# Kernel optimization log

Hardware: AMD Instinct MI355X
Metric: run time of the kernel (lower is better)

Reference implementation:

```python
import jax, jax.numpy as jnp
import numpy as np

PI = 3.141592653589793
TAU = 0.5          # gumbel-softmax temperature
EPS = 1e-6
B, N, D = 128, 32, 256

def _linear(x, w, b=None):
    y = x @ w.T
    return y if b is None else y + b

def _wrap(a):
    return (a + PI) % (2 * PI) - PI

def setup_inputs() -> dict:
    key = jax.random.key(0)
    ks = jax.random.split(key, 16)
    s = 0.05
    return {
        "embedding": jax.random.normal(ks[0], (B, N, 11), jnp.float32),
        "gumbel_u": jax.random.uniform(ks[1], (B * N, N - 1, 2), jnp.float32),
        "emb1_w": jax.random.normal(ks[2], (128, 5), jnp.float32) * s,
        "emb1_b": jnp.zeros((128,), jnp.float32),
        "emb2_w": jax.random.normal(ks[3], (D, 128), jnp.float32) * s,
        "emb2_b": jnp.zeros((D,), jnp.float32),
        "hm1_w": jax.random.normal(ks[4], (D, D + 7), jnp.float32) * s,
        "hm1_b": jnp.zeros((D,), jnp.float32),
        "hm2_w": jax.random.normal(ks[5], (D, D), jnp.float32) * s,
        "hm2_b": jnp.zeros((D,), jnp.float32),
        "he_w": jax.random.normal(ks[6], (2, D), jnp.float32) * s,
        "he_b": jnp.zeros((2,), jnp.float32),
        "q_w": jax.random.normal(ks[7], (D, D), jnp.float32) * s,
        "k_w": jax.random.normal(ks[8], (D, 10), jnp.float32) * s,
        "v_w": jax.random.normal(ks[9], (D, 10), jnp.float32) * s,
        "v_b": jnp.zeros((D,), jnp.float32),
        "dec_w": jax.random.normal(ks[10], (2 * D, 2 * D), jnp.float32) * s,
        "dec_b": jnp.zeros((2 * D,), jnp.float32),
    }

def reference(embedding, gumbel_u, emb1_w, emb1_b, emb2_w, emb2_b,
              hm1_w, hm1_b, hm2_w, hm2_b, he_w, he_b,
              q_w, k_w, v_w, v_b, dec_w, dec_b):
    b, n, _ = embedding.shape
    d = q_w.shape[0]
    # static off-diagonal index lists (i,j), j != i, row-major like mask indexing
    rows, cols = np.nonzero(~np.eye(n, dtype=bool))

    embed = embedding[:, :, 4:9].reshape(b * n, 5)
    position = embedding[:, :, :2]
    heading = embedding[:, :, 2:4]
    action = embedding[:, :, 7:9]
    goal = embedding[:, :, -2:]

    # agent embedding MLP (leaky_relu slope 0.01, torch default)
    h = jax.nn.leaky_relu(_linear(embed, emb1_w, emb1_b))
    agent_embed = jax.nn.leaky_relu(_linear(h, emb2_w, emb2_b)).reshape(b, n, d)

    # pairwise geometry  [b,i,j,...]
    rel_vec = position[:, None, :, :] - position[:, :, None, :]   # pos_j - pos_i
    dx, dy = rel_vec[..., 0], rel_vec[..., 1]
    rel_dist = jnp.linalg.norm(rel_vec, axis=-1, keepdims=True) / 12.0
    heading_angle_i = jnp.arctan2(heading[..., 1], heading[..., 0])[:, :, None]  # [b,n,1]
    angle = _wrap(jnp.arctan2(dy, dx) - heading_angle_i)
    hj_cos = jnp.broadcast_to(heading[:, None, :, 0], (b, n, n))
    hj_sin = jnp.broadcast_to(heading[:, None, :, 1], (b, n, n))
    action_j = jnp.broadcast_to(action[:, None, :, :], (b, n, n, 2))
    edge_features = jnp.concatenate([
        rel_dist, jnp.cos(angle)[..., None], jnp.sin(angle)[..., None],
        hj_cos[..., None], hj_sin[..., None], action_j], axis=-1)  # [b,n,n,7]

    # hard attention branch (off-diagonal pairs only)
    h_i_flat = jnp.broadcast_to(agent_embed[:, :, None, :], (b, n, n - 1, d)).reshape(b * n, n - 1, d)
    edge_flat = edge_features[:, rows, cols].reshape(b * n, n - 1, 7)
    hard_input = jnp.concatenate([h_i_flat, edge_flat], axis=-1)
    h_hard = _linear(jax.nn.relu(_linear(hard_input, hm1_w, hm1_b)), hm2_w, hm2_b)
    hard_logits = _linear(h_hard, he_w, he_b)                      # [b*n, n-1, 2]
    g = -jnp.log(-jnp.log(gumbel_u + 1e-10) + 1e-10)
    hard_soft = jax.nn.softmax((hard_logits + g) / TAU, axis=-1)
    hard_weights = hard_soft[..., 1].reshape(b, n, n - 1)

    unnorm = jnp.linalg.norm(rel_vec, axis=-1, keepdims=True)      # [b,n,n,1]
    unnorm_rel_dist = unnorm[:, rows, cols].reshape(b * n, n - 1, 1)

    # goal polar features
    goal_rel_vec = goal[:, None, :, :] - position[:, :, None, :]   # [b,n,n,2]
    goal_rel_dist = jnp.linalg.norm(goal_rel_vec, axis=-1, keepdims=True)
    goal_rel_angle = _wrap(jnp.arctan2(goal_rel_vec[..., 1], goal_rel_vec[..., 0]) - heading_angle_i)
    goal_polar = jnp.concatenate([goal_rel_dist, jnp.cos(goal_rel_angle)[..., None],
                                  jnp.sin(goal_rel_angle)[..., None]], axis=-1)
    soft_edge = jnp.concatenate([edge_features, goal_polar], axis=-1)  # [b,n,n,10]

    # soft attention (vectorized over agents; off-diagonal gather)
    q = agent_embed @ q_w.T                                         # [b,n,d]
    k = soft_edge @ k_w.T                                           # [b,n,n,d]
    v = jax.nn.relu(_linear(soft_edge, v_w, v_b))                   # [b,n,n,d]
    k_off = k[:, rows, cols].reshape(b, n, n - 1, d)
    v_off = v[:, rows, cols].reshape(b, n, n - 1, d)
    score = jnp.einsum('bnd,bnjd->bnj', q, k_off) / jnp.sqrt(jnp.float32(d))
    soft_w = jax.nn.softmax(score, axis=-1)
    combined = soft_w * hard_weights                                # [b,n,n-1]
    x = jnp.einsum('bnjd,bnj->bnd', v_off, combined).reshape(b * n, d)

    final_input = jnp.concatenate([agent_embed.reshape(b * n, d), x], axis=-1)
    output = _linear(final_input, dec_w, dec_b)                     # [b*n, 2d]

    cwn = combined / (combined.sum(axis=-1, keepdims=True) + EPS)
    mean_entropy = (-(cwn * jnp.log(cwn + EPS)).sum(axis=-1)).mean()
    comb_w = combined.reshape(n, -1)  # matches torch.stack(dim=1).reshape(n, -1)

    return (output, hard_logits[..., 1], unnorm_rel_dist, mean_entropy, hard_weights, comb_w)
```

## Files before the change

### kernel.cpp

```cpp
#include <hip/hip_runtime.h>
#include <hip/hip_bf16.h>
#include <math.h>

typedef __hip_bfloat16 bf16;
typedef short bf16x8 __attribute__((ext_vector_type(8)));
typedef float f32x4 __attribute__((ext_vector_type(4)));
typedef unsigned short u16;

#define R_TOT 4096
#define NJ 31

#define OFF_AE   0
#define OFF_QK   1048576
#define OFF_S1   2097152
#define OFF_ENT  4542464
#define OFF_X    4546560
#define OFF_W    5595136
#define W_E1W   0
#define W_E1B   640
#define W_E2P   768
#define W_E2B   33536
#define W_H1W   33792
#define W_H1B   101120
#define W_H2B   166912
#define W_HEW   167168
#define W_HEB   167680
#define W_W1EP  167684
#define W_HE2P  171780
#define W_CB    173828
#define W_S1P   200452
#define W_KW    233220
#define W_VW    235780
#define W_VB    238340
#define W_DECWT 238596
#define W_DECB  500740
#define W_QKM   501252

#define OUT0 0
#define OUT1 2097152
#define OUT2 2224128
#define OUT3 2351104
#define OUT4 2351105
#define OUT5 2478081

__device__ __forceinline__ float b2f(bf16 x) { return __bfloat162float(x); }
__device__ __forceinline__ float ldin(const void* p, int i, int flag) {
    return flag ? b2f(((const bf16*)p)[i]) : ((const float*)p)[i];
}
__device__ __forceinline__ void stout(void* p, int i, float v, int flag) {
    if (flag) ((bf16*)p)[i] = __float2bfloat16(v);
    else      ((float*)p)[i] = v;
}
__device__ __forceinline__ u16 f2bbits(float v) {
    bf16 h = __float2bfloat16(v);
    return *(u16*)&h;
}
__device__ __forceinline__ int detect_flag(const void* emb) {
    float x = ((const float*)emb)[threadIdx.x & 63];
    int sane = (x == x) && (fabsf(x) < 1e20f);
    unsigned long long m = __ballot(sane);
    return (__popcll(m) == 64) ? 0 : 1;
}

__global__ __launch_bounds__(256) void k_prep(
        const void* emb,
        const void* e1w, const void* e1b, const void* e2w, const void* e2b,
        const void* h1w, const void* h1b, const void* h2w, const void* h2b,
        const void* hew, const void* heb, const void* qw,  const void* kw,
        const void* vw,  const void* vb,  const void* decw,const void* decb,
        float* W) {
    int flag = detect_flag(emb);
    int blk = blockIdx.x;
    if (blk < 2048) {
        int idx = blk * 256 + threadIdx.x;
        if (idx < 262144) {
            int jj   = idx & 7;
            int lane = (idx >> 3) & 63;
            int tile = idx >> 9;
            int nt = tile & 31, kt = tile >> 5;
            int n = nt * 16 + (lane & 15);
            int k = kt * 32 + ((lane >> 4) << 3) + jj;
            ((u16*)(W + W_DECWT))[idx] = f2bbits(ldin(decw, n * 512 + k, flag));
        }
        int j = idx - 262144;
        if (j >= 0 && j < 98304) {
            int p;
            const void* src; int ldm, Wdst;
            if (j < 32768)      { p = j;          src = e2w; ldm = 128; Wdst = W_E2P; }
            else                { p = j - 32768;  src = h1w; ldm = 263; Wdst = W_S1P; }
            int jj   = p & 7;
            int lane = (p >> 3) & 63;
            int tile = p >> 9;
            int nt = tile & 15, kt = tile >> 4;
            int n = nt * 16 + (lane & 15);
            int k = kt * 32 + ((lane >> 4) << 3) + jj;
            ((u16*)(W + Wdst))[p] = f2bbits(ldin(src, n * ldm + k, flag));
        } else if (j >= 98304 && j < 174082) {
            int q2 = j - 98304;
            if      (q2 < 640)   W[W_E1W  + q2]           = ldin(e1w,  q2,          flag);
            else if (q2 < 768)   W[W_E1B  + (q2 - 640)]   = ldin(e1b,  q2 - 640,    flag);
            else if (q2 < 1024)  W[W_E2B  + (q2 - 768)]   = ldin(e2b,  q2 - 768,    flag);
            else if (q2 < 68352) W[W_H1W  + (q2 - 1024)]  = ldin(h1w,  q2 - 1024,   flag);
            else if (q2 < 68608) W[W_H1B  + (q2 - 68352)] = ldin(h1b,  q2 - 68352,  flag);
            else if (q2 < 68864) W[W_H2B  + (q2 - 68608)] = ldin(h2b,  q2 - 68608,  flag);
            else if (q2 < 69376) W[W_HEW  + (q2 - 68864)] = ldin(hew,  q2 - 68864,  flag);
            else if (q2 < 69378) W[W_HEB  + (q2 - 69376)] = ldin(heb,  q2 - 69376,  flag);
            else if (q2 < 71938) W[W_KW   + (q2 - 69378)] = ldin(kw,   q2 - 69378,  flag);
            else if (q2 < 74498) W[W_VW   + (q2 - 71938)] = ldin(vw,   q2 - 71938,  flag);
            else if (q2 < 74754) W[W_VB   + (q2 - 74498)] = ldin(vb,   q2 - 74498,  flag);
            else                 W[W_DECB + (q2 - 74754)] = ldin(decb, q2 - 74754,  flag);
        }
    } else if (blk < 2064) {
        int p = (blk - 2048) * 256 + threadIdx.x;
        int jj = p & 7, lane = (p >> 3) & 63, kt = p >> 9;
        int k = kt * 32 + ((lane >> 4) << 3) + jj;
        int n = lane & 15;
        float v = 0.f;
        if (n < 10) {
            for (int d = 0; d < 256; d++)
                v += ldin(qw, d * 256 + k, flag) * ldin(kw, d * 10 + n, flag);
        }
        ((u16*)(W + W_QKM))[p] = f2bbits(v);
    } else {
        int p = (blk - 2064) * 256 + threadIdx.x;
        if (p < 8192) {
            int jj = p & 7, lane = (p >> 3) & 63, nt = p >> 9;
            int n = nt * 16 + (lane & 15);
            int k = ((lane >> 4) << 3) + jj;
            float v = (k < 7) ? ldin(h1w, n * 263 + 256 + k, flag) : 0.f;
            ((u16*)(W + W_W1EP))[p] = f2bbits(v);
        } else if (p < 12288) {
            int q = p - 8192;
            int jj = q & 7, lane = (q >> 3) & 63, kt = q >> 9;
            int n = lane & 15;
            int c = kt * 32 + ((lane >> 4) << 3) + jj;
            float v = 0.f;
            if (n < 2) {
                for (int d = 0; d < 256; d++)
                    v += ldin(hew, n * 256 + d, flag) * ldin(h2w, d * 256 + c, flag);
            }
            ((u16*)(W + W_HE2P))[q] = f2bbits(v);
        } else if (p < 12290) {
            int i = p - 12288;
            float v = ldin(heb, i, flag);
            for (int d = 0; d < 256; d++)
                v += ldin(hew, i * 256 + d, flag) * ldin(h2b, d, flag);
            W[W_CB + i] = v;
        }
    }
}

__global__ __launch_bounds__(256) void k_embed(const void* emb, const float* W,
                                               u16* aeb, float* qkws, float* s1ws) {
    int flag = detect_flag(emb);
    int r0 = blockIdx.x * 16;
    __shared__ float embL[16][12];
    __shared__ u16 hB[16][136];
    __shared__ u16 aeB[16][264];
    int tid = threadIdx.x;
    for (int idx = tid; idx < 16 * 11; idx += 256) {
        int s = idx / 11, t = idx % 11;
        embL[s][t] = ldin(emb, (r0 + s) * 11 + t, flag);
    }
    __syncthreads();
    for (int idx = tid; idx < 16 * 128; idx += 256) {
        int s = idx >> 7, jo = idx & 127;
        float v = W[W_E1B + jo];
#pragma unroll
        for (int t = 0; t < 5; t++) v += W[W_E1W + jo * 5 + t] * embL[s][4 + t];
        hB[s][jo] = f2bbits(v > 0.f ? v : 0.01f * v);
    }
    __syncthreads();
    int wv = tid >> 6, ln = tid & 63;
    int lr = ln & 15, quad = ln >> 4;
    {
        const bf16x8* Bp = (const bf16x8*)(W + W_E2P);
        f32x4 acc[4];
#pragma unroll
        for (int nt = 0; nt < 4; nt++) acc[nt] = (f32x4){0.f, 0.f, 0.f, 0.f};
#pragma unroll
        for (int kt = 0; kt < 4; kt++) {
            bf16x8 af = *(const bf16x8*)&hB[lr][kt * 32 + (quad << 3)];
#pragma unroll
            for (int nt = 0; nt < 4; nt++) {
                bf16x8 bfr = Bp[(kt * 16 + (wv * 4 + nt)) * 64 + ln];
                acc[nt] = __builtin_amdgcn_mfma_f32_16x16x32_bf16(af, bfr, acc[nt], 0, 0, 0);
            }
        }
#pragma unroll
        for (int nt = 0; nt < 4; nt++) {
            int d = wv * 64 + nt * 16 + lr;
            float bias = W[W_E2B + d];
#pragma unroll
            for (int reg = 0; reg < 4; reg++) {
                int m = quad * 4 + reg;
                float v = acc[nt][reg] + bias;
                v = v > 0.f ? v : 0.01f * v;
                u16 bits = f2bbits(v);
                aeB[m][d] = bits;
                aeb[(r0 + m) * 256 + d] = bits;
            }
        }
    }
    __syncthreads();
    {
        const bf16x8* Bs = (const bf16x8*)(W + W_S1P);
        f32x4 sac[4];
#pragma unroll
        for (int nt = 0; nt < 4; nt++) sac[nt] = (f32x4){0.f, 0.f, 0.f, 0.f};
#pragma unroll
        for (int kt = 0; kt < 8; kt++) {
            bf16x8 af = *(const bf16x8*)&aeB[lr][kt * 32 + (quad << 3)];
#pragma unroll
            for (int nt = 0; nt < 4; nt++) {
                bf16x8 bs = Bs[(kt * 16 + (wv * 4 + nt)) * 64 + ln];
                sac[nt] = __builtin_amdgcn_mfma_f32_16x16x32_bf16(af, bs, sac[nt], 0, 0, 0);
            }
        }
#pragma unroll
        for (int nt = 0; nt < 4; nt++) {
            int d = wv * 64 + nt * 16 + lr;
            float bias = W[W_H1B + d];
#pragma unroll
            for (int reg = 0; reg < 4; reg++) {
                int m = quad * 4 + reg;
                s1ws[(r0 + m) * 256 + d] = sac[nt][reg] + bias;
            }
        }
        if (wv == 0) {
            const bf16x8* Bm = (const bf16x8*)(W + W_QKM);
            f32x4 qk = (f32x4){0.f, 0.f, 0.f, 0.f};
#pragma unroll
            for (int kt = 0; kt < 8; kt++) {
                bf16x8 af = *(const bf16x8*)&aeB[lr][kt * 32 + (quad << 3)];
                qk = __builtin_amdgcn_mfma_f32_16x16x32_bf16(af, Bm[kt * 64 + ln], qk, 0, 0, 0);
            }
            if (lr < 10) {
#pragma unroll
                for (int reg = 0; reg < 4; reg++) {
                    int m = quad * 4 + reg;
                    qkws[(r0 + m) * 10 + lr] = qk[reg];
                }
            }
        }
    }
}

__global__ __launch_bounds__(256) void k_fused(const void* emb, const void* gum,
                                               const float* s1ws, const float* qkws, const float* W,
                                               u16* xb, float* entws, void* out) {
    int flag = detect_flag(emb);
    int r = blockIdx.x;
    int b = r >> 5, i = r & 31;
    __shared__ float embB[32][12];
    __shared__ float seL[32][10];
    __shared__ u16 eA[32][32];
    __shared__ u16 a1[32][264];
    __shared__ float pj[4][32][2];
    __shared__ float cL[32];
    __shared__ float qkL[10];
    int tid = threadIdx.x;
    for (int idx = tid; idx < 32 * 11; idx += 256) {
        int s = idx / 11, t = idx % 11;
        embB[s][t] = ldin(emb, (b * 32 + s) * 11 + t, flag);
    }
    for (int idx = tid; idx < 32 * 32; idx += 256) ((u16*)eA)[idx] = 0;
    if (tid >= 64 && tid < 74) qkL[tid - 64] = qkws[r * 10 + (tid - 64)];
    __syncthreads();
    if (tid < NJ) {
        int jp = tid;
        int j = jp + (jp >= i ? 1 : 0);
        float pix = embB[i][0], piy = embB[i][1], hix = embB[i][2], hiy = embB[i][3];
        float pjx = embB[j][0], pjy = embB[j][1], hjx = embB[j][2], hjy = embB[j][3];
        float ajx = embB[j][7], ajy = embB[j][8];
        float gjx = embB[j][9], gjy = embB[j][10];
        float dx = pjx - pix, dy = pjy - piy;
        float dist = sqrtf(dx * dx + dy * dy);
        float hai = atan2f(hiy, hix);
        float ang = atan2f(dy, dx) - hai;
        float gx = gjx - pix, gy = gjy - piy;
        float gdist = sqrtf(gx * gx + gy * gy);
        float gang = atan2f(gy, gx) - hai;
        float f[10];
        f[0] = dist * (1.f / 12.f);
        f[1] = cosf(ang); f[2] = sinf(ang);
        f[3] = hjx; f[4] = hjy; f[5] = ajx; f[6] = ajy;
        f[7] = gdist; f[8] = cosf(gang); f[9] = sinf(gang);
#pragma unroll
        for (int t = 0; t < 10; t++) seL[jp][t] = f[t];
#pragma unroll
        for (int t = 0; t < 7; t++) eA[jp][t] = f2bbits(f[t]);
        stout(out, OUT2 + r * NJ + jp, dist, flag);
    }
    __syncthreads();
    int wv = tid >> 6, ln = tid & 63;
    int lr = ln & 15, quad = ln >> 4;
    {
        const bf16x8* Bp = (const bf16x8*)(W + W_W1EP);
        bf16x8 af0 = *(const bf16x8*)&eA[lr][quad << 3];
        bf16x8 af1 = *(const bf16x8*)&eA[16 + lr][quad << 3];
#pragma unroll
        for (int nt = 0; nt < 4; nt++) {
            int gnt = wv * 4 + nt;
            int d = gnt * 16 + lr;
            float s1v = s1ws[r * 256 + d];
            f32x4 acc0 = (f32x4){s1v, s1v, s1v, s1v};
            f32x4 acc1 = acc0;
            bf16x8 bb = Bp[gnt * 64 + ln];
            acc0 = __builtin_amdgcn_mfma_f32_16x16x32_bf16(af0, bb, acc0, 0, 0, 0);
            acc1 = __builtin_amdgcn_mfma_f32_16x16x32_bf16(af1, bb, acc1, 0, 0, 0);
#pragma unroll
            for (int reg = 0; reg < 4; reg++) {
                a1[(quad << 2) + reg][d]      = f2bbits(fmaxf(acc0[reg], 0.f));
                a1[16 + (quad << 2) + reg][d] = f2bbits(fmaxf(acc1[reg], 0.f));
            }
        }
    }
    __syncthreads();
    {
        const bf16x8* Ep = (const bf16x8*)(W + W_HE2P);
        f32x4 l0 = (f32x4){0.f, 0.f, 0.f, 0.f};
        f32x4 l1 = (f32x4){0.f, 0.f, 0.f, 0.f};
#pragma unroll
        for (int kk = 0; kk < 2; kk++) {
            int kt = wv * 2 + kk;
            bf16x8 a0 = *(const bf16x8*)&a1[lr][kt * 32 + (quad << 3)];
            bf16x8 a1f = *(const bf16x8*)&a1[16 + lr][kt * 32 + (quad << 3)];
            bf16x8 bb = Ep[kt * 64 + ln];
            l0 = __builtin_amdgcn_mfma_f32_16x16x32_bf16(a0, bb, l0, 0, 0, 0);
            l1 = __builtin_amdgcn_mfma_f32_16x16x32_bf16(a1f, bb, l1, 0, 0, 0);
        }
        if (lr < 2) {
#pragma unroll
            for (int reg = 0; reg < 4; reg++) {
                pj[wv][(quad << 2) + reg][lr]      = l0[reg];
                pj[wv][16 + (quad << 2) + reg][lr] = l1[reg];
            }
        }
    }
    __syncthreads();
    if (wv == 0) {
        float hwv = 0.f;
        if (ln < NJ) {
            float p0 = pj[0][ln][0] + pj[1][ln][0] + pj[2][ln][0] + pj[3][ln][0];
            float p1 = pj[0][ln][1] + pj[1][ln][1] + pj[2][ln][1] + pj[3][ln][1];
            float l0 = p0 + W[W_CB + 0], l1 = p1 + W[W_CB + 1];
            float u0 = ldin(gum, (r * NJ + ln) * 2 + 0, flag);
            float u1 = ldin(gum, (r * NJ + ln) * 2 + 1, flag);
            float g0 = -logf(-logf(u0 + 1e-10f) + 1e-10f);
            float g1 = -logf(-logf(u1 + 1e-10f) + 1e-10f);
            float dl = ((l1 + g1) - (l0 + g0)) * 2.0f;
            hwv = 1.f / (1.f + expf(-dl));
            stout(out, OUT1 + r * NJ + ln, l1, flag);
            stout(out, OUT4 + r * NJ + ln, hwv, flag);
        }
        float sc = -1e30f;
        if (ln < NJ) {
            float p = 0.f;
#pragma unroll
            for (int t = 0; t < 10; t++) p += qkL[t] * seL[ln][t];
            sc = p * (1.f / 16.f);
        }
        float m = sc;
#pragma unroll
        for (int s = 32; s >= 1; s >>= 1) m = fmaxf(m, __shfl_xor(m, s, 64));
        float e = (ln < NJ) ? expf(sc - m) : 0.f;
        float sum = e;
#pragma unroll
        for (int s = 32; s >= 1; s >>= 1) sum += __shfl_xor(sum, s, 64);
        float sw = e / sum;
        float cmb = sw * hwv;
        if (ln < NJ) {
            cL[ln] = cmb;
            stout(out, OUT5 + r * NJ + ln, cmb, flag);
        }
        float csum = cmb;
#pragma unroll
        for (int s = 32; s >= 1; s >>= 1) csum += __shfl_xor(csum, s, 64);
        float cwn = cmb / (csum + 1e-6f);
        float et = (ln < NJ) ? -cwn * logf(cwn + 1e-6f) : 0.f;
#pragma unroll
        for (int s = 32; s >= 1; s >>= 1) et += __shfl_xor(et, s, 64);
        if (ln == 0) entws[r] = et;
    }
    __syncthreads();
    float vwr[10];
#pragma unroll
    for (int t = 0; t < 10; t++) vwr[t] = W[W_VW + tid * 10 + t];
    float vbv = W[W_VB + tid];
    float x = 0.f;
    for (int j = 0; j < NJ; j++) {
        float v = vbv;
#pragma unroll
        for (int t = 0; t < 10; t++) v += vwr[t] * seL[j][t];
        v = fmaxf(v, 0.f);
        x += v * cL[j];
    }
    xb[r * 256 + tid] = f2bbits(x);
}

__global__ __launch_bounds__(256) void k_dec(const void* emb, const u16* aeb, const u16* xb,
                                             const float* W, void* out) {
    int flag = detect_flag(emb);
    int r0 = (blockIdx.x >> 2) * 32;
    int nq = blockIdx.x & 3;
    __shared__ u16 finB[32][520];
    int tid = threadIdx.x;
    for (int idx = tid; idx < 32 * 512; idx += 256) {
        int s = idx >> 9, c = idx & 511;
        finB[s][c] = (c < 256) ? aeb[(r0 + s) * 256 + c] : xb[(r0 + s) * 256 + (c - 256)];
    }
    __syncthreads();
    int wv = tid >> 6, ln = tid & 63;
    int lr = ln & 15, quad = ln >> 4;
    const bf16x8* Bp = (const bf16x8*)(W + W_DECWT);
    f32x4 acc[2][2];
#pragma unroll
    for (int mt = 0; mt < 2; mt++)
#pragma unroll
        for (int nt = 0; nt < 2; nt++) acc[mt][nt] = (f32x4){0.f, 0.f, 0.f, 0.f};
#pragma unroll
    for (int kt = 0; kt < 16; kt++) {
        bf16x8 af[2];
#pragma unroll
        for (int mt = 0; mt < 2; mt++)
            af[mt] = *(const bf16x8*)&finB[mt * 16 + lr][kt * 32 + (quad << 3)];
#pragma unroll
        for (int nt = 0; nt < 2; nt++) {
            int gnt = nq * 8 + wv * 2 + nt;
            bf16x8 bfr = Bp[(kt * 32 + gnt) * 64 + ln];
#pragma unroll
            for (int mt = 0; mt < 2; mt++)
                acc[mt][nt] = __builtin_amdgcn_mfma_f32_16x16x32_bf16(af[mt], bfr, acc[mt][nt], 0, 0, 0);
        }
    }
#pragma unroll
    for (int nt = 0; nt < 2; nt++) {
        int d = (nq * 8 + wv * 2 + nt) * 16 + lr;
        float bias = W[W_DECB + d];
#pragma unroll
        for (int mt = 0; mt < 2; mt++)
#pragma unroll
            for (int reg = 0; reg < 4; reg++) {
                int m = mt * 16 + quad * 4 + reg;
                stout(out, OUT0 + (r0 + m) * 512 + d, acc[mt][nt][reg] + bias, flag);
            }
    }
}

__global__ void k_ent(const void* emb, const float* entws, void* out) {
    int flag = detect_flag(emb);
    __shared__ float red[4];
    int tid = threadIdx.x;
    float s = 0.f;
    for (int i = tid; i < R_TOT; i += 256) s += entws[i];
#pragma unroll
    for (int m = 32; m >= 1; m >>= 1) s += __shfl_xor(s, m, 64);
    if ((tid & 63) == 0) red[tid >> 6] = s;
    __syncthreads();
    if (tid == 0) {
        float t = red[0] + red[1] + red[2] + red[3];
        stout(out, OUT3, t / (float)R_TOT, flag);
    }
}

extern "C" void kernel_launch(void* const* d_in, const int* in_sizes, int n_in,
                              void* d_out, int out_size, void* d_ws, size_t ws_size,
                              hipStream_t stream) {
    const void* emb  = d_in[0];
    const void* gum  = d_in[1];
    const void* e1w  = d_in[2];
    const void* e1b  = d_in[3];
    const void* e2w  = d_in[4];
    const void* e2b  = d_in[5];
    const void* h1w  = d_in[6];
    const void* h1b  = d_in[7];
    const void* h2w  = d_in[8];
    const void* h2b  = d_in[9];
    const void* hew  = d_in[10];
    const void* heb  = d_in[11];
    const void* qw   = d_in[12];
    const void* kw   = d_in[13];
    const void* vw   = d_in[14];
    const void* vb   = d_in[15];
    const void* decw = d_in[16];
    const void* decb = d_in[17];

    float* wsf = (float*)d_ws;
    u16*   aeb  = (u16*)(wsf + OFF_AE);
    float* qkws = wsf + OFF_QK;
    float* s1ws = wsf + OFF_S1;
    float* entw = wsf + OFF_ENT;
    u16*   xb   = (u16*)(wsf + OFF_X);
    float* W    = wsf + OFF_W;

    hipLaunchKernelGGL(k_prep, dim3(2113), dim3(256), 0, stream,
                       emb, e1w, e1b, e2w, e2b, h1w, h1b, h2w, h2b, hew, heb,
                       qw, kw, vw, vb, decw, decb, W);
    hipLaunchKernelGGL(k_embed, dim3(256), dim3(256), 0, stream, emb, W, aeb, qkws, s1ws);
    hipLaunchKernelGGL(k_fused, dim3(4096), dim3(256), 0, stream,
                       emb, gum, s1ws, qkws, W, xb, entw, d_out);
    hipLaunchKernelGGL(k_dec, dim3(512), dim3(256), 0, stream, emb, aeb, xb, W, d_out);
    hipLaunchKernelGGL(k_ent, dim3(1), dim3(256), 0, stream, emb, entw, d_out);
}
```

Before: 186.0 us.

## Parallelize prep dot products across lanes, drop unused weight copies, fold entropy into decoder

The serial 256-term dot products in k_prep (the Q·K weight fold, the head-edge fold with h2w, and the bias fold) now run split across 16 lanes per output and are combined with shuffle reductions. This gives more parallel work and shorter per-thread loops. Weight copies that are never read (h1w, h2b, hew, heb, kw) are no longer written. The entropy mean reduction moves into block 0 of k_dec, removing one kernel launch, at the cost of extra tail work in that one block.

```diff
diff --git a/kernel.cpp b/kernel.cpp
--- a/kernel.cpp
+++ b/kernel.cpp
@@ -20,16 +20,11 @@
 #define W_E1B   640
 #define W_E2P   768
 #define W_E2B   33536
-#define W_H1W   33792
 #define W_H1B   101120
-#define W_H2B   166912
-#define W_HEW   167168
-#define W_HEB   167680
 #define W_W1EP  167684
 #define W_HE2P  171780
 #define W_CB    173828
 #define W_S1P   200452
-#define W_KW    233220
 #define W_VW    235780
 #define W_VB    238340
 #define W_DECWT 238596
@@ -71,8 +66,9 @@
         float* W) {
     int flag = detect_flag(emb);
     int blk = blockIdx.x;
+    int tid = threadIdx.x;
     if (blk < 2048) {
-        int idx = blk * 256 + threadIdx.x;
+        int idx = blk * 256 + tid;
         if (idx < 262144) {
             int jj   = idx & 7;
             int lane = (idx >> 3) & 63;
@@ -95,57 +91,69 @@
             int n = nt * 16 + (lane & 15);
             int k = kt * 32 + ((lane >> 4) << 3) + jj;
             ((u16*)(W + Wdst))[p] = f2bbits(ldin(src, n * ldm + k, flag));
-        } else if (j >= 98304 && j < 174082) {
+        } else if (j >= 98304 && j < 102912) {
             int q2 = j - 98304;
             if      (q2 < 640)   W[W_E1W  + q2]           = ldin(e1w,  q2,          flag);
             else if (q2 < 768)   W[W_E1B  + (q2 - 640)]   = ldin(e1b,  q2 - 640,    flag);
             else if (q2 < 1024)  W[W_E2B  + (q2 - 768)]   = ldin(e2b,  q2 - 768,    flag);
-            else if (q2 < 68352) W[W_H1W  + (q2 - 1024)]  = ldin(h1w,  q2 - 1024,   flag);
-            else if (q2 < 68608) W[W_H1B  + (q2 - 68352)] = ldin(h1b,  q2 - 68352,  flag);
-            else if (q2 < 68864) W[W_H2B  + (q2 - 68608)] = ldin(h2b,  q2 - 68608,  flag);
-            else if (q2 < 69376) W[W_HEW  + (q2 - 68864)] = ldin(hew,  q2 - 68864,  flag);
-            else if (q2 < 69378) W[W_HEB  + (q2 - 69376)] = ldin(heb,  q2 - 69376,  flag);
-            else if (q2 < 71938) W[W_KW   + (q2 - 69378)] = ldin(kw,   q2 - 69378,  flag);
-            else if (q2 < 74498) W[W_VW   + (q2 - 71938)] = ldin(vw,   q2 - 71938,  flag);
-            else if (q2 < 74754) W[W_VB   + (q2 - 74498)] = ldin(vb,   q2 - 74498,  flag);
-            else                 W[W_DECB + (q2 - 74754)] = ldin(decb, q2 - 74754,  flag);
-        }
-    } else if (blk < 2064) {
-        int p = (blk - 2048) * 256 + threadIdx.x;
+            else if (q2 < 1280)  W[W_H1B  + (q2 - 1024)]  = ldin(h1b,  q2 - 1024,   flag);
+            else if (q2 < 3840)  W[W_VW   + (q2 - 1280)]  = ldin(vw,   q2 - 1280,   flag);
+            else if (q2 < 4096)  W[W_VB   + (q2 - 3840)]  = ldin(vb,   q2 - 3840,   flag);
+            else                 W[W_DECB + (q2 - 4096)]  = ldin(decb, q2 - 4096,   flag);
+        }
+    } else if (blk < 2304) {
+        int p = (blk - 2048) * 16 + (tid >> 4);
+        int l = tid & 15;
         int jj = p & 7, lane = (p >> 3) & 63, kt = p >> 9;
         int k = kt * 32 + ((lane >> 4) << 3) + jj;
         int n = lane & 15;
         float v = 0.f;
         if (n < 10) {
-            for (int d = 0; d < 256; d++)
+#pragma unroll
+            for (int dd = 0; dd < 16; dd++) {
+                int d = l + 16 * dd;
                 v += ldin(qw, d * 256 + k, flag) * ldin(kw, d * 10 + n, flag);
-        }
-        ((u16*)(W + W_QKM))[p] = f2bbits(v);
+            }
+        }
+        v += __shfl_xor(v, 1, 64); v += __shfl_xor(v, 2, 64);
+        v += __shfl_xor(v, 4, 64); v += __shfl_xor(v, 8, 64);
+        if (l == 0) ((u16*)(W + W_QKM))[p] = f2bbits(v);
+    } else if (blk < 2560) {
+        int q = (blk - 2304) * 16 + (tid >> 4);
+        int l = tid & 15;
+        int jj = q & 7, lane = (q >> 3) & 63, kt = q >> 9;
+        int n = lane & 15;
+        int c = kt * 32 + ((lane >> 4) << 3) + jj;
+        float v = 0.f;
+        if (n < 2) {
+#pragma unroll
+            for (int dd = 0; dd < 16; dd++) {
+                int d = l + 16 * dd;
+                v += ldin(hew, n * 256 + d, flag) * ldin(h2w, d * 256 + c, flag);
+            }
+        }
+        v += __shfl_xor(v, 1, 64); v += __shfl_xor(v, 2, 64);
+        v += __shfl_xor(v, 4, 64); v += __shfl_xor(v, 8, 64);
+        if (l == 0) ((u16*)(W + W_HE2P))[q] = f2bbits(v);
+    } else if (blk < 2592) {
+        int p = (blk - 2560) * 256 + tid;
+        int jj = p & 7, lane = (p >> 3) & 63, nt = p >> 9;
+        int n = nt * 16 + (lane & 15);
+        int k = ((lane >> 4) << 3) + jj;
+        float v = (k < 7) ? ldin(h1w, n * 263 + 256 + k, flag) : 0.f;
+        ((u16*)(W + W_W1EP))[p] = f2bbits(v);
     } else {
-        int p = (blk - 2064) * 256 + threadIdx.x;
-        if (p < 8192) {
-            int jj = p & 7, lane = (p >> 3) & 63, nt = p >> 9;
-            int n = nt * 16 + (lane & 15);
-            int k = ((lane >> 4) << 3) + jj;
-            float v = (k < 7) ? ldin(h1w, n * 263 + 256 + k, flag) : 0.f;
-            ((u16*)(W + W_W1EP))[p] = f2bbits(v);
-        } else if (p < 12288) {
-            int q = p - 8192;
-            int jj = q & 7, lane = (q >> 3) & 63, kt = q >> 9;
-            int n = lane & 15;
-            int c = kt * 32 + ((lane >> 4) << 3) + jj;
+        if (tid < 32) {
+            int i = tid >> 4, l = tid & 15;
             float v = 0.f;
-            if (n < 2) {
-                for (int d = 0; d < 256; d++)
-                    v += ldin(hew, n * 256 + d, flag) * ldin(h2w, d * 256 + c, flag);
-            }
-            ((u16*)(W + W_HE2P))[q] = f2bbits(v);
-        } else if (p < 12290) {
-            int i = p - 12288;
-            float v = ldin(heb, i, flag);
-            for (int d = 0; d < 256; d++)
+#pragma unroll
+            for (int dd = 0; dd < 16; dd++) {
+                int d = l + 16 * dd;
                 v += ldin(hew, i * 256 + d, flag) * ldin(h2b, d, flag);
-            W[W_CB + i] = v;
+            }
+            v += __shfl_xor(v, 1, 64); v += __shfl_xor(v, 2, 64);
+            v += __shfl_xor(v, 4, 64); v += __shfl_xor(v, 8, 64);
+            if (l == 0) W[W_CB + i] = v + ldin(heb, i, flag);
         }
     }
 }
@@ -400,7 +408,7 @@
 }
 
 __global__ __launch_bounds__(256) void k_dec(const void* emb, const u16* aeb, const u16* xb,
-                                             const float* W, void* out) {
+                                             const float* W, const float* entws, void* out) {
     int flag = detect_flag(emb);
     int r0 = (blockIdx.x >> 2) * 32;
     int nq = blockIdx.x & 3;
@@ -446,21 +454,18 @@
                 stout(out, OUT0 + (r0 + m) * 512 + d, acc[mt][nt][reg] + bias, flag);
             }
     }
-}
-
-__global__ void k_ent(const void* emb, const float* entws, void* out) {
-    int flag = detect_flag(emb);
-    __shared__ float red[4];
-    int tid = threadIdx.x;
-    float s = 0.f;
-    for (int i = tid; i < R_TOT; i += 256) s += entws[i];
-#pragma unroll
-    for (int m = 32; m >= 1; m >>= 1) s += __shfl_xor(s, m, 64);
-    if ((tid & 63) == 0) red[tid >> 6] = s;
-    __syncthreads();
-    if (tid == 0) {
-        float t = red[0] + red[1] + red[2] + red[3];
-        stout(out, OUT3, t / (float)R_TOT, flag);
+    if (blockIdx.x == 0) {
+        __shared__ float red[4];
+        float s = 0.f;
+        for (int i2 = tid; i2 < R_TOT; i2 += 256) s += entws[i2];
+#pragma unroll
+        for (int m = 32; m >= 1; m >>= 1) s += __shfl_xor(s, m, 64);
+        if ((tid & 63) == 0) red[tid >> 6] = s;
+        __syncthreads();
+        if (tid == 0) {
+            float t = red[0] + red[1] + red[2] + red[3];
+            stout(out, OUT3, t / (float)R_TOT, flag);
+        }
     }
 }
 
@@ -494,12 +499,11 @@
     u16*   xb   = (u16*)(wsf + OFF_X);
     float* W    = wsf + OFF_W;
 
-    hipLaunchKernelGGL(k_prep, dim3(2113), dim3(256), 0, stream,
+    hipLaunchKernelGGL(k_prep, dim3(2593), dim3(256), 0, stream,
                        emb, e1w, e1b, e2w, e2b, h1w, h1b, h2w, h2b, hew, heb,
                        qw, kw, vw, vb, decw, decb, W);
     hipLaunchKernelGGL(k_embed, dim3(256), dim3(256), 0, stream, emb, W, aeb, qkws, s1ws);
     hipLaunchKernelGGL(k_fused, dim3(4096), dim3(256), 0, stream,
                        emb, gum, s1ws, qkws, W, xb, entw, d_out);
-    hipLaunchKernelGGL(k_dec, dim3(512), dim3(256), 0, stream, emb, aeb, xb, W, d_out);
-    hipLaunchKernelGGL(k_ent, dim3(1), dim3(256), 0, stream, emb, entw, d_out);
-}
+    hipLaunchKernelGGL(k_dec, dim3(512), dim3(256), 0, stream, emb, aeb, xb, W, entw, d_out);
+}
```

After: 161.1 us. -13.3%, faster.
